# Kernel optimization log

Hardware: AMD Instinct MI355X
Metric: run time of the kernel (lower is better)

The kernel has to match this reference:

```python
import jax, jax.numpy as jnp
import numpy as np

B, CW_DIM = 256, 8192
DIM_EMBED = 128
DICT_SIZE = 4096
DIM_CODES = CW_DIM // DIM_EMBED  # 64


def setup_inputs() -> dict:
    key = jax.random.key(0)
    k1, k2 = jax.random.split(key)
    x = jax.random.normal(k1, (B, CW_DIM), dtype=jnp.float32)
    dictionary = jax.random.normal(k2, (DIM_CODES, DICT_SIZE, DIM_EMBED), dtype=jnp.float32)
    return {"x": x, "dictionary": dictionary}


def reference(x, dictionary):
    """VQVAE.quantise (eval mode): pairwise sq-distance -> argmin -> gather + one-hot.

    x: [B, cw_dim], dictionary: [C, S, E] with cw_dim = C*E.
    Returns (cw_embed [B, C*E], one_hot_idx [B, C, S]).
    """
    Bb, D = x.shape
    C, S, E = dictionary.shape
    xr = x.reshape(Bb, C, E)                                   # [B, C, E]
    x_sq = jnp.sum(xr * xr, axis=-1, keepdims=True)            # [B, C, 1]
    d_sq = jnp.sum(dictionary * dictionary, axis=-1)           # [C, S]
    cross = jnp.einsum('bce,cse->bcs', xr, dictionary)         # [B, C, S] (GEMM)
    dist = x_sq + d_sq[None, :, :] - 2.0 * cross               # [B, C, S]
    idx = jnp.argmin(dist, axis=-1)                            # [B, C]
    # gather nearest codes: dictionary[c, idx[b,c]] -> [B, C, E]
    code_ids = jnp.arange(C)[None, :]                          # [1, C]
    cw_embed = dictionary[code_ids, idx]                       # [B, C, E]
    cw_embed = cw_embed.reshape(Bb, C * E)                     # [B, cw_dim]
    one_hot_idx = jax.nn.one_hot(idx, S, dtype=x.dtype)        # [B, C, S]
    return cw_embed, one_hot_idx
```

## Files before the change

kernel.cpp:

```cpp
#include <hip/hip_runtime.h>
#include <stdint.h>


#define B_SZ 256
#define C_SZ 64
#define E_SZ 128
#define S_SZ 4096
#define CW   8192
#define TS   64
#define SPB  1024
#define LDB  128

typedef __attribute__((ext_vector_type(4))) float    float4a;
typedef __attribute__((ext_vector_type(8))) _Float16 half8;

__device__ __forceinline__ int swz(int row, int cf16) {
    return row * LDB + (cf16 ^ ((row & 7) << 3));
}

__device__ __forceinline__ void split8(float4a f0, float4a f1, half8& hi, half8& lo) {
    #pragma unroll
    for (int j = 0; j < 4; ++j) {
        _Float16 h0 = (_Float16)f0[j];
        hi[j]     = h0;
        lo[j]     = (_Float16)(f0[j] - (float)h0);
        _Float16 h1 = (_Float16)f1[j];
        hi[4 + j] = h1;
        lo[4 + j] = (_Float16)(f1[j] - (float)h1);
    }
}

__global__ __launch_bounds__(512, 2) void argmin_mfma(
    const float* __restrict__ x,
    const float* __restrict__ dict,
    float* __restrict__ cw_out,
    float* __restrict__ oh)
{
    __shared__ __attribute__((aligned(16))) _Float16 bh[2][TS * LDB];
    __shared__ __attribute__((aligned(16))) _Float16 bl[2][TS * LDB];
    __shared__ __attribute__((aligned(16))) float dsqp[2][TS][8];
    float* rv = reinterpret_cast<float*>(bh);
    int*   ri = reinterpret_cast<int*>(bl);

    const int tid   = threadIdx.x;
    const int lane  = tid & 63;
    const int quad  = lane >> 4;
    const int l15   = lane & 15;
    const int wid   = tid >> 6;
    const int mq    = wid & 3;
    const int nh    = wid >> 2;
    const int c     = blockIdx.x & 63;
    const int squad = blockIdx.x >> 6;
    const int sbase = squad * SPB;

    int m_attr[4], n_attr[4];
    {
        half8 ones, enc;
        #pragma unroll
        for (int j = 0; j < 8; ++j) { ones[j] = (_Float16)1.0f; enc[j] = (_Float16)(float)l15; }
        float4a z = {0.f, 0.f, 0.f, 0.f};
        float4a pr = __builtin_amdgcn_mfma_f32_16x16x32_f16(enc, ones, z, 0, 0, 0);
        float4a pc = __builtin_amdgcn_mfma_f32_16x16x32_f16(ones, enc, z, 0, 0, 0);
        #pragma unroll
        for (int r = 0; r < 4; ++r) {
            m_attr[r] = (int)(pr[r] * 0.03125f + 0.5f);
            n_attr[r] = (int)(pc[r] * 0.03125f + 0.5f);
        }
    }

    half8 ah[4][4], al[4][4];
    #pragma unroll
    for (int mi = 0; mi < 4; ++mi) {
        int b = mq * 64 + mi * 16 + l15;
        const float* xr = x + (size_t)b * CW + c * E_SZ;
        #pragma unroll
        for (int kk = 0; kk < 4; ++kk) {
            float4a f0 = *reinterpret_cast<const float4a*>(xr + kk * 32 + quad * 8);
            float4a f1 = *reinterpret_cast<const float4a*>(xr + kk * 32 + quad * 8 + 4);
            split8(f0, f1, ah[mi][kk], al[mi][kk]);
        }
    }

    const int srow = tid >> 3;
    const int kq   = (tid & 7) * 16;
    const int q8   = tid & 7;
    const float* drow = dict + ((size_t)c * S_SZ + sbase + srow) * E_SZ + kq;

    float4a pf[4];
    #pragma unroll
    for (int ck = 0; ck < 4; ++ck)
        pf[ck] = *reinterpret_cast<const float4a*>(drow + ck * 4);
    {
        float dp = 0.f;
        #pragma unroll
        for (int ck = 0; ck < 2; ++ck) {
            half8 h, l;
            split8(pf[2 * ck], pf[2 * ck + 1], h, l);
            #pragma unroll
            for (int j = 0; j < 4; ++j) {
                dp = fmaf(pf[2 * ck][j], pf[2 * ck][j], dp);
                dp = fmaf(pf[2 * ck + 1][j], pf[2 * ck + 1][j], dp);
            }
            *reinterpret_cast<half8*>(&bh[0][swz(srow, kq + ck * 8)]) = h;
            *reinterpret_cast<half8*>(&bl[0][swz(srow, kq + ck * 8)]) = l;
        }
        dsqp[0][srow][q8] = dp;
    }

    float bestv[16];
    int   besti[16];
    #pragma unroll
    for (int i = 0; i < 16; ++i) { bestv[i] = 3.4e38f; besti[i] = 0; }

    __syncthreads();

    int cur = 0;
    for (int it = 0; it < 16; ++it) {
        if (it + 1 < 16) {
            const float* dr = drow + (size_t)(it + 1) * (TS * E_SZ);
            #pragma unroll
            for (int ck = 0; ck < 4; ++ck)
                pf[ck] = *reinterpret_cast<const float4a*>(dr + ck * 4);
        }

        {
            const int zrow = it * 16 + (tid >> 5);
            const int t5   = tid & 31;
            float* zb = oh + ((size_t)zrow * C_SZ + c) * S_SZ + sbase;
            float4a zz = {0.f, 0.f, 0.f, 0.f};
            #pragma unroll
            for (int j = 0; j < 8; ++j)
                __builtin_nontemporal_store(zz, reinterpret_cast<float4a*>(zb) + t5 + j * 32);
        }

        const _Float16* bhc = bh[cur];
        const _Float16* blc = bl[cur];
        float4a acc[4][2] = {{{0.f,0.f,0.f,0.f},{0.f,0.f,0.f,0.f}},
                             {{0.f,0.f,0.f,0.f},{0.f,0.f,0.f,0.f}},
                             {{0.f,0.f,0.f,0.f},{0.f,0.f,0.f,0.f}},
                             {{0.f,0.f,0.f,0.f},{0.f,0.f,0.f,0.f}}};
        __builtin_amdgcn_s_setprio(1);
        #pragma unroll
        for (int kk = 0; kk < 4; ++kk) {
            half8 bhf[2], blf[2];
            #pragma unroll
            for (int ni = 0; ni < 2; ++ni) {
                const int sl = nh * 32 + ni * 16 + l15;
                bhf[ni] = *reinterpret_cast<const half8*>(bhc + swz(sl, kk * 32 + quad * 8));
                blf[ni] = *reinterpret_cast<const half8*>(blc + swz(sl, kk * 32 + quad * 8));
            }
            #pragma unroll
            for (int mi = 0; mi < 4; ++mi)
                #pragma unroll
                for (int ni = 0; ni < 2; ++ni) {
                    acc[mi][ni] = __builtin_amdgcn_mfma_f32_16x16x32_f16(
                        ah[mi][kk], bhf[ni], acc[mi][ni], 0, 0, 0);
                    acc[mi][ni] = __builtin_amdgcn_mfma_f32_16x16x32_f16(
                        ah[mi][kk], blf[ni], acc[mi][ni], 0, 0, 0);
                    acc[mi][ni] = __builtin_amdgcn_mfma_f32_16x16x32_f16(
                        al[mi][kk], bhf[ni], acc[mi][ni], 0, 0, 0);
                }
        }
        __builtin_amdgcn_s_setprio(0);

        #pragma unroll
        for (int ni = 0; ni < 2; ++ni)
            #pragma unroll
            for (int r = 0; r < 4; ++r) {
                const int sl = nh * 32 + ni * 16 + n_attr[r];
                float4a qa = *reinterpret_cast<const float4a*>(&dsqp[cur][sl][0]);
                float4a qb = *reinterpret_cast<const float4a*>(&dsqp[cur][sl][4]);
                float dsq = ((qa[0] + qa[1]) + (qa[2] + qa[3]))
                          + ((qb[0] + qb[1]) + (qb[2] + qb[3]));
                int sg = sbase + it * TS + sl;
                #pragma unroll
                for (int mi = 0; mi < 4; ++mi) {
                    float dist = dsq - 2.0f * acc[mi][ni][r];
                    int slot = mi * 4 + r;
                    if (dist < bestv[slot]) { bestv[slot] = dist; besti[slot] = sg; }
                }
            }

        if (it + 1 < 16) {
            const int nb = cur ^ 1;
            float dp = 0.f;
            #pragma unroll
            for (int ck = 0; ck < 2; ++ck) {
                half8 h, l;
                split8(pf[2 * ck], pf[2 * ck + 1], h, l);
                #pragma unroll
                for (int j = 0; j < 4; ++j) {
                    dp = fmaf(pf[2 * ck][j], pf[2 * ck][j], dp);
                    dp = fmaf(pf[2 * ck + 1][j], pf[2 * ck + 1][j], dp);
                }
                *reinterpret_cast<half8*>(&bh[nb][swz(srow, kq + ck * 8)]) = h;
                *reinterpret_cast<half8*>(&bl[nb][swz(srow, kq + ck * 8)]) = l;
            }
            dsqp[nb][srow][q8] = dp;
        }
        __syncthreads();
        cur ^= 1;
    }


    #pragma unroll
    for (int mi = 0; mi < 4; ++mi)
        #pragma unroll
        for (int r = 0; r < 4; ++r) {
            int row = mq * 64 + mi * 16 + m_attr[r];
            int col = nh * 16 + n_attr[r];
            rv[col * 256 + row] = bestv[mi * 4 + r];
            ri[col * 256 + row] = besti[mi * 4 + r];
        }
    __syncthreads();

    if (tid < 256) {
        float bv = 3.4e38f; int bi = 0x7fffffff;
        #pragma unroll 4
        for (int j = 0; j < 32; ++j) {
            float v = rv[j * 256 + tid];
            int   i = ri[j * 256 + tid];
            if (v < bv || (v == bv && i < bi)) { bv = v; bi = i; }
        }
        float* cp = cw_out + (size_t)tid * CW + c * E_SZ + squad * 2;
        cp[0] = bv;
        cp[1] = __int_as_float(bi);
    }
}

__global__ __launch_bounds__(256) void finalize(
    const float* __restrict__ dict,
    float* __restrict__ cw_out,
    float* __restrict__ oh)
{
    __shared__ int fid[64];
    const int c     = blockIdx.x & 63;
    const int btile = blockIdx.x >> 6;
    const int tid   = threadIdx.x;

    if (tid < 64) {
        const int row = btile * 64 + tid;
        const float* cp = cw_out + (size_t)row * CW + c * E_SZ;
        float bv = cp[0]; int bi = __float_as_int(cp[1]);
        #pragma unroll
        for (int k = 1; k < 4; ++k) {
            float v = cp[2 * k];
            if (v < bv) { bv = v; bi = __float_as_int(cp[2 * k + 1]); }
        }
        fid[tid] = bi;
        oh[((size_t)row * C_SZ + c) * S_SZ + bi] = 1.0f;
    }
    __syncthreads();

    const int row = tid >> 2, q = tid & 3;
    const int bi = fid[row];
    const float4a* src = reinterpret_cast<const float4a*>(
        dict + ((size_t)c * S_SZ + bi) * E_SZ) + q * 8;
    float4a* dst = reinterpret_cast<float4a*>(
        cw_out + (size_t)(btile * 64 + row) * CW + c * E_SZ) + q * 8;
    #pragma unroll
    for (int j = 0; j < 8; ++j) dst[j] = src[j];
}

extern "C" void kernel_launch(void* const* d_in, const int* in_sizes, int n_in,
                              void* d_out, int out_size, void* d_ws, size_t ws_size,
                              hipStream_t stream) {
    const float* x    = (const float*)d_in[0];
    const float* dict = (const float*)d_in[1];
    float* out = (float*)d_out;
    float* oh  = out + (size_t)B_SZ * CW;

    argmin_mfma<<<dim3(256), dim3(512), 0, stream>>>(x, dict, out, oh);
    finalize<<<dim3(256), dim3(256), 0, stream>>>(dict, out, oh);
}
```

Measured before the change: 437.3 us.

## Reshape warp tiling to 32x128 per wave with 128-code tiles

Doubles the dictionary tile to 128 codes per iteration, halving the loop count and the number of block barriers. Each of the 8 waves now owns 32 batch rows across all 128 codes instead of 64 rows by 32 codes. The same B fragment is reused across the wave's two M subtiles, which changes the LDS read-to-MFMA ratio and per-thread register use. It also doubles LDS use per block, which at launch bound (512,2) may limit occupancy, and it halves the dsq partial sums and the final reduction width.

```diff
diff --git a/kernel.cpp b/kernel.cpp
--- a/kernel.cpp
+++ b/kernel.cpp
@@ -7,8 +7,9 @@
 #define E_SZ 128
 #define S_SZ 4096
 #define CW   8192
-#define TS   64
+#define TS   128
 #define SPB  1024
+#define NIT  (SPB / TS)
 #define LDB  128
 
 typedef __attribute__((ext_vector_type(4))) float    float4a;
@@ -38,7 +39,7 @@
 {
     __shared__ __attribute__((aligned(16))) _Float16 bh[2][TS * LDB];
     __shared__ __attribute__((aligned(16))) _Float16 bl[2][TS * LDB];
-    __shared__ __attribute__((aligned(16))) float dsqp[2][TS][8];
+    __shared__ __attribute__((aligned(16))) float dsqp[2][TS][4];
     float* rv = reinterpret_cast<float*>(bh);
     int*   ri = reinterpret_cast<int*>(bl);
 
@@ -46,9 +47,7 @@
     const int lane  = tid & 63;
     const int quad  = lane >> 4;
     const int l15   = lane & 15;
-    const int wid   = tid >> 6;
-    const int mq    = wid & 3;
-    const int nh    = wid >> 2;
+    const int mq    = tid >> 6;
     const int c     = blockIdx.x & 63;
     const int squad = blockIdx.x >> 6;
     const int sbase = squad * SPB;
@@ -68,10 +67,10 @@
         }
     }
 
-    half8 ah[4][4], al[4][4];
-    #pragma unroll
-    for (int mi = 0; mi < 4; ++mi) {
-        int b = mq * 64 + mi * 16 + l15;
+    half8 ah[2][4], al[2][4];
+    #pragma unroll
+    for (int mi = 0; mi < 2; ++mi) {
+        int b = mq * 32 + mi * 16 + l15;
         const float* xr = x + (size_t)b * CW + c * E_SZ;
         #pragma unroll
         for (int kk = 0; kk < 4; ++kk) {
@@ -81,19 +80,19 @@
         }
     }
 
-    const int srow = tid >> 3;
-    const int kq   = (tid & 7) * 16;
-    const int q8   = tid & 7;
+    const int srow = tid >> 2;
+    const int kq   = (tid & 3) * 32;
+    const int q4   = tid & 3;
     const float* drow = dict + ((size_t)c * S_SZ + sbase + srow) * E_SZ + kq;
 
-    float4a pf[4];
-    #pragma unroll
-    for (int ck = 0; ck < 4; ++ck)
+    float4a pf[8];
+    #pragma unroll
+    for (int ck = 0; ck < 8; ++ck)
         pf[ck] = *reinterpret_cast<const float4a*>(drow + ck * 4);
     {
         float dp = 0.f;
         #pragma unroll
-        for (int ck = 0; ck < 2; ++ck) {
+        for (int ck = 0; ck < 4; ++ck) {
             half8 h, l;
             split8(pf[2 * ck], pf[2 * ck + 1], h, l);
             #pragma unroll
@@ -104,88 +103,85 @@
             *reinterpret_cast<half8*>(&bh[0][swz(srow, kq + ck * 8)]) = h;
             *reinterpret_cast<half8*>(&bl[0][swz(srow, kq + ck * 8)]) = l;
         }
-        dsqp[0][srow][q8] = dp;
-    }
-
-    float bestv[16];
-    int   besti[16];
-    #pragma unroll
-    for (int i = 0; i < 16; ++i) { bestv[i] = 3.4e38f; besti[i] = 0; }
+        dsqp[0][srow][q4] = dp;
+    }
+
+    float bestv[8];
+    int   besti[8];
+    #pragma unroll
+    for (int i = 0; i < 8; ++i) { bestv[i] = 3.4e38f; besti[i] = 0; }
 
     __syncthreads();
 
     int cur = 0;
-    for (int it = 0; it < 16; ++it) {
-        if (it + 1 < 16) {
+    for (int it = 0; it < NIT; ++it) {
+        if (it + 1 < NIT) {
             const float* dr = drow + (size_t)(it + 1) * (TS * E_SZ);
             #pragma unroll
-            for (int ck = 0; ck < 4; ++ck)
+            for (int ck = 0; ck < 8; ++ck)
                 pf[ck] = *reinterpret_cast<const float4a*>(dr + ck * 4);
         }
 
         {
-            const int zrow = it * 16 + (tid >> 5);
-            const int t5   = tid & 31;
+            const int zrow = it * 32 + (tid >> 4);
+            const int t4   = tid & 15;
             float* zb = oh + ((size_t)zrow * C_SZ + c) * S_SZ + sbase;
             float4a zz = {0.f, 0.f, 0.f, 0.f};
             #pragma unroll
-            for (int j = 0; j < 8; ++j)
-                __builtin_nontemporal_store(zz, reinterpret_cast<float4a*>(zb) + t5 + j * 32);
+            for (int j = 0; j < 16; ++j)
+                __builtin_nontemporal_store(zz, reinterpret_cast<float4a*>(zb) + t4 + j * 16);
         }
 
         const _Float16* bhc = bh[cur];
         const _Float16* blc = bl[cur];
-        float4a acc[4][2] = {{{0.f,0.f,0.f,0.f},{0.f,0.f,0.f,0.f}},
-                             {{0.f,0.f,0.f,0.f},{0.f,0.f,0.f,0.f}},
-                             {{0.f,0.f,0.f,0.f},{0.f,0.f,0.f,0.f}},
-                             {{0.f,0.f,0.f,0.f},{0.f,0.f,0.f,0.f}}};
+        float4a acc[2][8];
+        #pragma unroll
+        for (int mi = 0; mi < 2; ++mi)
+            #pragma unroll
+            for (int ni = 0; ni < 8; ++ni)
+                acc[mi][ni] = (float4a){0.f, 0.f, 0.f, 0.f};
         __builtin_amdgcn_s_setprio(1);
         #pragma unroll
         for (int kk = 0; kk < 4; ++kk) {
-            half8 bhf[2], blf[2];
-            #pragma unroll
-            for (int ni = 0; ni < 2; ++ni) {
-                const int sl = nh * 32 + ni * 16 + l15;
-                bhf[ni] = *reinterpret_cast<const half8*>(bhc + swz(sl, kk * 32 + quad * 8));
-                blf[ni] = *reinterpret_cast<const half8*>(blc + swz(sl, kk * 32 + quad * 8));
-            }
-            #pragma unroll
-            for (int mi = 0; mi < 4; ++mi)
+            #pragma unroll
+            for (int ni = 0; ni < 8; ++ni) {
+                const int sl = ni * 16 + l15;
+                half8 bhf = *reinterpret_cast<const half8*>(bhc + swz(sl, kk * 32 + quad * 8));
+                half8 blf = *reinterpret_cast<const half8*>(blc + swz(sl, kk * 32 + quad * 8));
                 #pragma unroll
-                for (int ni = 0; ni < 2; ++ni) {
+                for (int mi = 0; mi < 2; ++mi) {
                     acc[mi][ni] = __builtin_amdgcn_mfma_f32_16x16x32_f16(
-                        ah[mi][kk], bhf[ni], acc[mi][ni], 0, 0, 0);
+                        ah[mi][kk], bhf, acc[mi][ni], 0, 0, 0);
                     acc[mi][ni] = __builtin_amdgcn_mfma_f32_16x16x32_f16(
-                        ah[mi][kk], blf[ni], acc[mi][ni], 0, 0, 0);
+                        ah[mi][kk], blf, acc[mi][ni], 0, 0, 0);
                     acc[mi][ni] = __builtin_amdgcn_mfma_f32_16x16x32_f16(
-                        al[mi][kk], bhf[ni], acc[mi][ni], 0, 0, 0);
+                        al[mi][kk], bhf, acc[mi][ni], 0, 0, 0);
                 }
+            }
         }
         __builtin_amdgcn_s_setprio(0);
 
         #pragma unroll
-        for (int ni = 0; ni < 2; ++ni)
+        for (int ni = 0; ni < 8; ++ni)
             #pragma unroll
             for (int r = 0; r < 4; ++r) {
-                const int sl = nh * 32 + ni * 16 + n_attr[r];
+                const int sl = ni * 16 + n_attr[r];
                 float4a qa = *reinterpret_cast<const float4a*>(&dsqp[cur][sl][0]);
-                float4a qb = *reinterpret_cast<const float4a*>(&dsqp[cur][sl][4]);
-                float dsq = ((qa[0] + qa[1]) + (qa[2] + qa[3]))
-                          + ((qb[0] + qb[1]) + (qb[2] + qb[3]));
+                float dsq = (qa[0] + qa[1]) + (qa[2] + qa[3]);
                 int sg = sbase + it * TS + sl;
                 #pragma unroll
-                for (int mi = 0; mi < 4; ++mi) {
+                for (int mi = 0; mi < 2; ++mi) {
                     float dist = dsq - 2.0f * acc[mi][ni][r];
                     int slot = mi * 4 + r;
                     if (dist < bestv[slot]) { bestv[slot] = dist; besti[slot] = sg; }
                 }
             }
 
-        if (it + 1 < 16) {
+        if (it + 1 < NIT) {
             const int nb = cur ^ 1;
             float dp = 0.f;
             #pragma unroll
-            for (int ck = 0; ck < 2; ++ck) {
+            for (int ck = 0; ck < 4; ++ck) {
                 half8 h, l;
                 split8(pf[2 * ck], pf[2 * ck + 1], h, l);
                 #pragma unroll
@@ -196,7 +192,7 @@
                 *reinterpret_cast<half8*>(&bh[nb][swz(srow, kq + ck * 8)]) = h;
                 *reinterpret_cast<half8*>(&bl[nb][swz(srow, kq + ck * 8)]) = l;
             }
-            dsqp[nb][srow][q8] = dp;
+            dsqp[nb][srow][q4] = dp;
         }
         __syncthreads();
         cur ^= 1;
@@ -204,11 +200,11 @@
 
 
     #pragma unroll
-    for (int mi = 0; mi < 4; ++mi)
+    for (int mi = 0; mi < 2; ++mi)
         #pragma unroll
         for (int r = 0; r < 4; ++r) {
-            int row = mq * 64 + mi * 16 + m_attr[r];
-            int col = nh * 16 + n_attr[r];
+            int row = mq * 32 + mi * 16 + m_attr[r];
+            int col = n_attr[r];
             rv[col * 256 + row] = bestv[mi * 4 + r];
             ri[col * 256 + row] = besti[mi * 4 + r];
         }
@@ -217,7 +213,7 @@
     if (tid < 256) {
         float bv = 3.4e38f; int bi = 0x7fffffff;
         #pragma unroll 4
-        for (int j = 0; j < 32; ++j) {
+        for (int j = 0; j < 16; ++j) {
             float v = rv[j * 256 + tid];
             int   i = ri[j * 256 + tid];
             if (v < bv || (v == bv && i < bi)) { bv = v; bi = i; }
```

New measurement: 485.7 us. +11.1%, slower.

## Stage dictionary tiles with direct global-to-LDS loads and split fp16 at consume time

Applied to the files above, without the earlier changes.

Replaces the register-staged prefetch, which converted dictionary rows to hi/lo fp16 and stored them into swizzled LDS, with async global_load_lds of raw fp32 tiles into an XOR-swizzled LDS buffer. Each MFMA wave now reads fp32 from LDS, splits it into hi/lo fp16 and computes the dictionary row norms itself, reducing them with shuffles. The aim is to take the global-load register round trip and the conversion work off the critical path and free registers. The cost is that the split and norm work is repeated by every wave that reads the same rows, and the LDS reads are twice as wide. The s_setprio hints are also dropped.

```diff
diff --git a/kernel.cpp b/kernel.cpp
--- a/kernel.cpp
+++ b/kernel.cpp
@@ -9,14 +9,12 @@
 #define CW   8192
 #define TS   64
 #define SPB  1024
-#define LDB  128
 
 typedef __attribute__((ext_vector_type(4))) float    float4a;
 typedef __attribute__((ext_vector_type(8))) _Float16 half8;
 
-__device__ __forceinline__ int swz(int row, int cf16) {
-    return row * LDB + (cf16 ^ ((row & 7) << 3));
-}
+typedef __attribute__((address_space(1))) const uint32_t gu32;
+typedef __attribute__((address_space(3))) uint32_t       lu32;
 
 __device__ __forceinline__ void split8(float4a f0, float4a f1, half8& hi, half8& lo) {
     #pragma unroll
@@ -36,11 +34,9 @@
     float* __restrict__ cw_out,
     float* __restrict__ oh)
 {
-    __shared__ __attribute__((aligned(16))) _Float16 bh[2][TS * LDB];
-    __shared__ __attribute__((aligned(16))) _Float16 bl[2][TS * LDB];
-    __shared__ __attribute__((aligned(16))) float dsqp[2][TS][8];
-    float* rv = reinterpret_cast<float*>(bh);
-    int*   ri = reinterpret_cast<int*>(bl);
+    __shared__ __attribute__((aligned(16))) float df[2][TS * E_SZ];
+    float* rv = reinterpret_cast<float*>(df[0]);
+    int*   ri = reinterpret_cast<int*>(df[1]);
 
     const int tid   = threadIdx.x;
     const int lane  = tid & 63;
@@ -81,47 +77,36 @@
         }
     }
 
-    const int srow = tid >> 3;
-    const int kq   = (tid & 7) * 16;
-    const int q8   = tid & 7;
-    const float* drow = dict + ((size_t)c * S_SZ + sbase + srow) * E_SZ + kq;
-
-    float4a pf[4];
-    #pragma unroll
-    for (int ck = 0; ck < 4; ++ck)
-        pf[ck] = *reinterpret_cast<const float4a*>(drow + ck * 4);
-    {
-        float dp = 0.f;
-        #pragma unroll
-        for (int ck = 0; ck < 2; ++ck) {
-            half8 h, l;
-            split8(pf[2 * ck], pf[2 * ck + 1], h, l);
-            #pragma unroll
-            for (int j = 0; j < 4; ++j) {
-                dp = fmaf(pf[2 * ck][j], pf[2 * ck][j], dp);
-                dp = fmaf(pf[2 * ck + 1][j], pf[2 * ck + 1][j], dp);
-            }
-            *reinterpret_cast<half8*>(&bh[0][swz(srow, kq + ck * 8)]) = h;
-            *reinterpret_cast<half8*>(&bl[0][swz(srow, kq + ck * 8)]) = l;
-        }
-        dsqp[0][srow][q8] = dp;
-    }
+    const char* dict_c = reinterpret_cast<const char*>(dict);
+    const size_t tile_gbyte0 = ((size_t)c * S_SZ + sbase) * E_SZ * 4;
+
+    auto STAGE = [&](int nb, int t) {
+        const char* gb = dict_c + tile_gbyte0 + (size_t)t * (TS * E_SZ * 4);
+        char* lb = reinterpret_cast<char*>(&df[nb][0]);
+        #pragma unroll
+        for (int k = 0; k < 4; ++k) {
+            const int off = wid * 4096 + k * 1024 + lane * 16;
+            const int row = off >> 9;
+            const int g   = (off >> 4) & 31;
+            const int src = row * 512 + ((g ^ (row & 7)) << 4);
+            __builtin_amdgcn_global_load_lds(
+                (gu32*)(gb + src),
+                (lu32*)(lb + wid * 4096 + k * 1024),
+                16, 0, 0);
+        }
+    };
 
     float bestv[16];
     int   besti[16];
     #pragma unroll
     for (int i = 0; i < 16; ++i) { bestv[i] = 3.4e38f; besti[i] = 0; }
 
+    STAGE(0, 0);
     __syncthreads();
 
     int cur = 0;
     for (int it = 0; it < 16; ++it) {
-        if (it + 1 < 16) {
-            const float* dr = drow + (size_t)(it + 1) * (TS * E_SZ);
-            #pragma unroll
-            for (int ck = 0; ck < 4; ++ck)
-                pf[ck] = *reinterpret_cast<const float4a*>(dr + ck * 4);
-        }
+        if (it + 1 < 16) STAGE(cur ^ 1, it + 1);
 
         {
             const int zrow = it * 16 + (tid >> 5);
@@ -133,21 +118,29 @@
                 __builtin_nontemporal_store(zz, reinterpret_cast<float4a*>(zb) + t5 + j * 32);
         }
 
-        const _Float16* bhc = bh[cur];
-        const _Float16* blc = bl[cur];
+        const char* dfc = reinterpret_cast<const char*>(&df[cur][0]);
         float4a acc[4][2] = {{{0.f,0.f,0.f,0.f},{0.f,0.f,0.f,0.f}},
                              {{0.f,0.f,0.f,0.f},{0.f,0.f,0.f,0.f}},
                              {{0.f,0.f,0.f,0.f},{0.f,0.f,0.f,0.f}},
                              {{0.f,0.f,0.f,0.f},{0.f,0.f,0.f,0.f}}};
-        __builtin_amdgcn_s_setprio(1);
+        float dp[2] = {0.f, 0.f};
         #pragma unroll
         for (int kk = 0; kk < 4; ++kk) {
             half8 bhf[2], blf[2];
             #pragma unroll
             for (int ni = 0; ni < 2; ++ni) {
                 const int sl = nh * 32 + ni * 16 + l15;
-                bhf[ni] = *reinterpret_cast<const half8*>(bhc + swz(sl, kk * 32 + quad * 8));
-                blf[ni] = *reinterpret_cast<const half8*>(blc + swz(sl, kk * 32 + quad * 8));
+                const int g0 = kk * 8 + quad * 2;
+                float4a f0 = *reinterpret_cast<const float4a*>(
+                    dfc + sl * 512 + (((g0)     ^ (sl & 7)) << 4));
+                float4a f1 = *reinterpret_cast<const float4a*>(
+                    dfc + sl * 512 + (((g0 + 1) ^ (sl & 7)) << 4));
+                split8(f0, f1, bhf[ni], blf[ni]);
+                #pragma unroll
+                for (int j = 0; j < 4; ++j) {
+                    dp[ni] = fmaf(f0[j], f0[j], dp[ni]);
+                    dp[ni] = fmaf(f1[j], f1[j], dp[ni]);
+                }
             }
             #pragma unroll
             for (int mi = 0; mi < 4; ++mi)
@@ -161,43 +154,29 @@
                         al[mi][kk], bhf[ni], acc[mi][ni], 0, 0, 0);
                 }
         }
-        __builtin_amdgcn_s_setprio(0);
+
+        float dsq[2];
+        #pragma unroll
+        for (int ni = 0; ni < 2; ++ni) {
+            float t = dp[ni] + __shfl_xor(dp[ni], 16, 64);
+            dsq[ni] = t + __shfl_xor(t, 32, 64);
+        }
 
         #pragma unroll
         for (int ni = 0; ni < 2; ++ni)
             #pragma unroll
             for (int r = 0; r < 4; ++r) {
-                const int sl = nh * 32 + ni * 16 + n_attr[r];
-                float4a qa = *reinterpret_cast<const float4a*>(&dsqp[cur][sl][0]);
-                float4a qb = *reinterpret_cast<const float4a*>(&dsqp[cur][sl][4]);
-                float dsq = ((qa[0] + qa[1]) + (qa[2] + qa[3]))
-                          + ((qb[0] + qb[1]) + (qb[2] + qb[3]));
-                int sg = sbase + it * TS + sl;
+                const int na = n_attr[r];
+                const float dv = __shfl(dsq[ni], (lane & 48) | na, 64);
+                const int sg = sbase + it * TS + nh * 32 + ni * 16 + na;
                 #pragma unroll
                 for (int mi = 0; mi < 4; ++mi) {
-                    float dist = dsq - 2.0f * acc[mi][ni][r];
+                    float dist = dv - 2.0f * acc[mi][ni][r];
                     int slot = mi * 4 + r;
                     if (dist < bestv[slot]) { bestv[slot] = dist; besti[slot] = sg; }
                 }
             }
 
-        if (it + 1 < 16) {
-            const int nb = cur ^ 1;
-            float dp = 0.f;
-            #pragma unroll
-            for (int ck = 0; ck < 2; ++ck) {
-                half8 h, l;
-                split8(pf[2 * ck], pf[2 * ck + 1], h, l);
-                #pragma unroll
-                for (int j = 0; j < 4; ++j) {
-                    dp = fmaf(pf[2 * ck][j], pf[2 * ck][j], dp);
-                    dp = fmaf(pf[2 * ck + 1][j], pf[2 * ck + 1][j], dp);
-                }
-                *reinterpret_cast<half8*>(&bh[nb][swz(srow, kq + ck * 8)]) = h;
-                *reinterpret_cast<half8*>(&bl[nb][swz(srow, kq + ck * 8)]) = l;
-            }
-            dsqp[nb][srow][q8] = dp;
-        }
         __syncthreads();
         cur ^= 1;
     }
```

Measured after the change: 407.6 us. 1.07x faster.
